# Kernel tuning notes

Hardware: AMD Instinct MI355X
Metric: run time of the kernel (lower is better)

The kernel has to match this reference:

```python
import jax, jax.numpy as jnp
import numpy as np

N = 16        # state dim n
M = 8         # control dim m
T = 50        # time_steps
DT = 0.01     # delta_t
SQRT_DT = DT ** 0.5
GAMMA = 0.1
SIGMA = 0.2
TAU = 0.5
H = 10        # hidden width of subnets
BATCH = 32768


def _mlp(params, x):
    W1, b1, W2, b2, W3, b3 = params
    h = jnp.tanh(x @ W1 + b1)
    h = jnp.tanh(h @ W2 + b2)
    return h @ W3 + b3


def setup_inputs() -> dict:
    key = jax.random.key(0)
    ks = jax.random.split(key, 32)

    def dense(k, i, o):
        return (jax.random.normal(k, (i, o), jnp.float32) / np.float32(np.sqrt(i)))

    inp = {
        'dw': jax.random.normal(ks[0], (T, BATCH, 1), jnp.float32) * SQRT_DT,
        'X0': jax.random.uniform(ks[1], (BATCH, N), jnp.float32),
        'A': dense(ks[2], N, N),
        'Bmat': dense(ks[3], N, M),
        'Cmat': dense(ks[4], N, N),
        'Dmat': dense(ks[5], N, M),
        # phi: (n+1) -> 10 -> 10 -> m
        'phi_W1': dense(ks[6], N + 1, H), 'phi_b1': jnp.zeros((H,), jnp.float32),
        'phi_W2': dense(ks[7], H, H),     'phi_b2': jnp.zeros((H,), jnp.float32),
        'phi_W3': dense(ks[8], H, M),     'phi_b3': jnp.zeros((M,), jnp.float32),
        # Z: (n+1) -> 10 -> 10 -> n
        'Z_W1': dense(ks[9], N + 1, H),   'Z_b1': jnp.zeros((H,), jnp.float32),
        'Z_W2': dense(ks[10], H, H),      'Z_b2': jnp.zeros((H,), jnp.float32),
        'Z_W3': dense(ks[11], H, N),      'Z_b3': jnp.zeros((N,), jnp.float32),
        # Y0: n -> 10 -> 10 -> n
        'Y0_W1': dense(ks[12], N, H),     'Y0_b1': jnp.zeros((H,), jnp.float32),
        'Y0_W2': dense(ks[13], H, H),     'Y0_b2': jnp.zeros((H,), jnp.float32),
        'Y0_W3': dense(ks[14], H, N),     'Y0_b3': jnp.zeros((N,), jnp.float32),
    }
    return inp


def reference(dw, X0, A, Bmat, Cmat, Dmat,
              phi_W1, phi_b1, phi_W2, phi_b2, phi_W3, phi_b3,
              Z_W1, Z_b1, Z_W2, Z_b2, Z_W3, Z_b3,
              Y0_W1, Y0_b1, Y0_W2, Y0_b2, Y0_W3, Y0_b3):
    phi_p = (phi_W1, phi_b1, phi_W2, phi_b2, phi_W3, phi_b3)
    Z_p = (Z_W1, Z_b1, Z_W2, Z_b2, Z_W3, Z_b3)
    Y0_p = (Y0_W1, Y0_b1, Y0_W2, Y0_b2, Y0_W3, Y0_b3)

    B = X0.shape[0]
    Y = _mlp(Y0_p, X0)                              # [B, n]
    t_grid = jnp.arange(T, dtype=X0.dtype) * DT     # [T]
    w_trap = jnp.ones((T,), X0.dtype).at[1:-1].set(2.0)  # trapezoid weights

    def step(carry, xs):
        X, Yc, lc = carry
        dwi, t, w = xs                              # dwi: [B,1]
        state = jnp.concatenate(
            [jnp.broadcast_to(t, (B, 1)).astype(X.dtype), X], axis=1)  # [B, n+1]
        Zv = _mlp(Z_p, state)                       # [B, n]
        u = _mlp(phi_p, state)                      # [B, m] (project = identity)
        # b_mult(M, x) == x @ M.T
        drift_X = X @ A.T + u @ Bmat.T + GAMMA      # [B, n]
        diffusion_X = X @ Cmat.T + u @ Dmat.T + SIGMA
        drift_Y = -(Yc @ A + Zv @ Cmat + X)         # f_x(X,u) = X
        # stop_recording branch: gradient of dH / pre_phi
        dH = Yc @ Bmat + Zv @ Dmat + u              # f_u(X,u) = u -> [B, m]
        pre_phi = jax.lax.stop_gradient(u - TAU * dH)
        Xn = X + drift_X * DT + dwi * diffusion_X
        Yn = Yc + drift_Y * DT + dwi * Zv
        lc = lc + 0.5 * DT * w * jnp.sum(jnp.square(u - pre_phi), axis=1)
        return (Xn, Yn, lc), None

    init = (X0, Y, jnp.zeros((B,), X0.dtype))
    (X, Y, loss_control), _ = jax.lax.scan(step, init, (dw, t_grid, w_trap))
    loss_bsde = jnp.sum(jnp.square(Y - X), axis=1)  # g_x(X) = X
    return jnp.stack([jnp.mean(loss_bsde), jnp.mean(loss_control)])
```

## Files before the change

### kernel.cpp

```cpp
#include <hip/hip_runtime.h>

namespace {

typedef float v4f __attribute__((ext_vector_type(4)));
typedef _Float16 half4 __attribute__((ext_vector_type(4)));
typedef __fp16 fp16x2 __attribute__((ext_vector_type(2)));
typedef unsigned int uint32;

constexpr int   kB     = 32768;
constexpr int   kT     = 50;
constexpr float kDT    = 0.01f;
constexpr float kGamma = 0.1f;
constexpr float kSigma = 0.2f;
constexpr float kTau   = 0.5f;
constexpr float kA     = 2.8853900817779268f;

constexpr int kNFrag      = 25;
constexpr int kFragDwords = kNFrag * 128;
constexpr int kBiasFloats = 13 * 16;

__device__ __forceinline__ float fexp2(float x) {
#if __has_builtin(__builtin_amdgcn_exp2f)
  return __builtin_amdgcn_exp2f(x);
#else
  return exp2f(x);
#endif
}

__device__ __forceinline__ float fact(float x) {
  return __builtin_amdgcn_rcpf(fexp2(x) + 1.0f);
}

__device__ __forceinline__ v4f act4(v4f a) {
  v4f r;
  r[0] = fact(a[0]); r[1] = fact(a[1]);
  r[2] = fact(a[2]); r[3] = fact(a[3]);
  return r;
}

__device__ __forceinline__ uint32 pk2rtn(float a, float b) {
  union { _Float16 h[2]; uint32 u; } z;
  z.h[0] = (_Float16)a; z.h[1] = (_Float16)b;
  return z.u;
}

__global__ __launch_bounds__(64) void prep_kernel(
    const float* __restrict__ A,   const float* __restrict__ Bm,
    const float* __restrict__ Cm,  const float* __restrict__ Dm,
    const float* __restrict__ pW1, const float* __restrict__ pb1,
    const float* __restrict__ pW2, const float* __restrict__ pb2,
    const float* __restrict__ pW3, const float* __restrict__ pb3,
    const float* __restrict__ zW1, const float* __restrict__ zb1,
    const float* __restrict__ zW2, const float* __restrict__ zb2,
    const float* __restrict__ zW3, const float* __restrict__ zb3,
    const float* __restrict__ yW1, const float* __restrict__ yb1,
    const float* __restrict__ yW2, const float* __restrict__ yb2,
    const float* __restrict__ yW3, const float* __restrict__ yb3,
    uint32* __restrict__ ws)
{
  const int tid = threadIdx.x;
  const int blk = blockIdx.x;

  auto sum10 = [](const float* W, int stride, int mm) {
    float s = 0.f;
#pragma unroll
    for (int j = 0; j < 10; ++j) s += W[j * stride + mm];
    return s;
  };

  if (blk < kNFrag) {
    const int m = tid & 15, q = tid >> 4;
    const int p = blk;

    auto comp = [&](const float* W1, const float* M, int ncol, int k,
                    float scale) -> float {
      if (m >= 10 || k >= ncol) return 0.f;
      float s = 0.f;
#pragma unroll
      for (int i = 0; i < 16; ++i) s += W1[(i + 1) * 10 + m] * M[i * ncol + k];
      return kA * scale * s;
    };

    auto wv = [&](int k) -> float {
      switch (p) {
        case 0:  return (m < 10) ? kA * yW1[k * 10 + m] : 0.f;
        case 1:  return (m < 10 && k < 10) ? -2.f * kA * yW2[k * 10 + m] : 0.f;
        case 2:  return (k < 10) ? -2.f * yW3[k * 16 + m] : 0.f;
        case 3:  return (m < 10) ? kA * zW1[(k + 1) * 10 + m] : 0.f;
        case 4:  return (m < 10) ? kA * pW1[(k + 1) * 10 + m] : 0.f;
        case 5:  return (m < 10 && k < 10) ? -2.f * kA * zW2[k * 10 + m] : 0.f;
        case 6:  return (m < 10 && k < 10) ? -2.f * kA * pW2[k * 10 + m] : 0.f;
        case 7:  return (k < 10) ? -2.f * zW3[k * 16 + m] : 0.f;
        case 8:  return (m < 8 && k < 10) ? -2.f * pW3[k * 8 + m] : 0.f;
        case 9:  return A[m * 16 + k];
        case 10: return (k < 8) ? Bm[m * 8 + k] : 0.f;
        case 11: return Cm[m * 16 + k];
        case 12: return (k < 8) ? Dm[m * 8 + k] : 0.f;
        case 13: return A[k * 16 + m];
        case 14: return Cm[k * 16 + m];
        case 15: return (m < 8) ? Bm[k * 8 + m] : 0.f;
        case 16: return (m < 8) ? Dm[k * 8 + m] : 0.f;
        case 17: return comp(zW1, A,  16, k, kDT);
        case 18: return comp(zW1, Cm, 16, k, 1.f);
        case 19: return comp(zW1, Bm,  8, k, kDT);
        case 20: return comp(zW1, Dm,  8, k, 1.f);
        case 21: return comp(pW1, A,  16, k, kDT);
        case 22: return comp(pW1, Cm, 16, k, 1.f);
        case 23: return comp(pW1, Bm,  8, k, kDT);
        case 24: return comp(pW1, Dm,  8, k, 1.f);
      }
      return 0.f;
    };

    const int k0 = 4 * q;
    ws[p * 128 + tid * 2]     = pk2rtn(wv(k0),     wv(k0 + 1));
    ws[p * 128 + tid * 2 + 1] = pk2rtn(wv(k0 + 2), wv(k0 + 3));
  } else {
    float* bsf = (float*)(ws + kFragDwords);
    auto sumx = [&](const float* W1, int mm) {
      float s = 0.f;
#pragma unroll
      for (int i = 0; i < 16; ++i) s += W1[(i + 1) * 10 + mm];
      return kA * s;
    };
    auto bval = [&](int a, int mm) -> float {
      const bool m10 = mm < 10;
      switch (a) {
        case 0:  return m10 ? kA * yb1[mm] : 0.f;
        case 1:  return m10 ? kA * (yb2[mm] + sum10(yW2, 10, mm)) : 0.f;
        case 2:  return yb3[mm] + sum10(yW3, 16, mm);
        case 3:  return m10 ? kA * (zb2[mm] + sum10(zW2, 10, mm)) : 0.f;
        case 4:  return m10 ? kA * (pb2[mm] + sum10(pW2, 10, mm)) : 0.f;
        case 5:  return zb3[mm] + sum10(zW3, 16, mm);
        case 6:  return (mm < 8) ? pb3[mm] + sum10(pW3, 8, mm) : 0.f;
        case 7:  return m10 ? kA * zW1[mm] : 0.f;
        case 8:  return m10 ? kA * zb1[mm] : 0.f;
        case 9:  return m10 ? kA * pW1[mm] : 0.f;
        case 10: return m10 ? kA * pb1[mm] : 0.f;
        case 11: return m10 ? sumx(zW1, mm) : 0.f;
        case 12: return m10 ? sumx(pW1, mm) : 0.f;
      }
      return 0.f;
    };
    for (int j = tid; j < kBiasFloats; j += 64) {
      bsf[j] = bval(j >> 4, j & 15);
    }
  }
}

__global__ __launch_bounds__(64)
__attribute__((amdgpu_waves_per_eu(2, 2)))
void bsde_kernel(const float* __restrict__ dw, const float* __restrict__ X0,
                 const uint32* __restrict__ wsu, float* __restrict__ out)
{
  const int lane = threadIdx.x;
  const int col  = lane & 15;
  const int quad = lane >> 4;
  const int e    = blockIdx.x * 16 + col;
  const int bq   = quad * 4;

  half4 af[kNFrag];
#pragma unroll
  for (int p = 0; p < kNFrag; ++p) {
    union { uint2 u; half4 h; } z;
    z.u = *(const uint2*)(wsu + p * 128 + lane * 2);
    af[p] = z.h;
  }

  const float* bsf = (const float*)(wsu + kFragDwords);
  const v4f c2z  = *(const v4f*)&bsf[3 * 16 + bq];
  const v4f c2p  = *(const v4f*)&bsf[4 * 16 + bq];
  const v4f c3z  = *(const v4f*)&bsf[5 * 16 + bq];
  const v4f c3p  = *(const v4f*)&bsf[6 * 16 + bq];
  const v4f vtz  = *(const v4f*)&bsf[7 * 16 + bq];
  const v4f vbz  = *(const v4f*)&bsf[8 * 16 + bq];
  const v4f vtp  = *(const v4f*)&bsf[9 * 16 + bq];
  const v4f vbp  = *(const v4f*)&bsf[10 * 16 + bq];
  const v4f w1sz = *(const v4f*)&bsf[11 * 16 + bq];
  const v4f w1sp = *(const v4f*)&bsf[12 * 16 + bq];

  auto pk4 = [](v4f a) -> half4 {
    union { fp16x2 p[2]; half4 h; } z;
    z.p[0] = __builtin_amdgcn_cvt_pkrtz(a[0], a[1]);
    z.p[1] = __builtin_amdgcn_cvt_pkrtz(a[2], a[3]);
    return z.h;
  };
  auto mm4 = [](half4 a, half4 b, v4f c) -> v4f {
    return __builtin_amdgcn_mfma_f32_16x16x16f16(a, b, c, 0, 0, 0);
  };

  const v4f gam4  = {kGamma, kGamma, kGamma, kGamma};
  const v4f sig4  = {kSigma, kSigma, kSigma, kSigma};
  const v4f zero4 = {0.f, 0.f, 0.f, 0.f};

  v4f x4 = *(const v4f*)&X0[e * 16 + bq];
  half4 xB = pk4(x4);
  v4f y4;
  {
    const v4f cy1 = *(const v4f*)&bsf[0 * 16 + bq];
    const v4f cy2 = *(const v4f*)&bsf[1 * 16 + bq];
    const v4f cy3 = *(const v4f*)&bsf[2 * 16 + bq];
    v4f h = mm4(af[0], xB, cy1);
    v4f g = mm4(af[1], pk4(act4(h)), cy2);
    y4    = mm4(af[2], pk4(act4(g)), cy3);
  }
  v4f hzp = mm4(af[3], xB, vbz);
  v4f hpp = mm4(af[4], xB, vbp);

  float dwv = dw[e];
  v4f xs0;
#pragma unroll
  for (int r = 0; r < 4; ++r) xs0[r] = x4[r] * dwv;
  half4 xDB = pk4(xs0);

  float lcp = 0.0f;

#pragma unroll 1
  for (int t = 0; t < kT; ++t) {
    const float dwn = (t < kT - 1) ? dw[(t + 1) * kB + e] : 0.0f;
    const float tvn = (float)(t + 1) * kDT;
    const float wt  = (t == 0 || t == kT - 1) ? 1.0f : 2.0f;

    half4 yB = pk4(y4);

    v4f dx1 = mm4(af[9],  xB, gam4);
    v4f fx1 = mm4(af[11], xB, sig4);
    v4f dy1 = mm4(af[13], yB, x4);
    v4f dh1 = mm4(af[15], yB, zero4);

    const float gs = kDT * kGamma + dwv * kSigma;
    v4f Cz, Cp;
#pragma unroll
    for (int r = 0; r < 4; ++r) {
      Cz[r] = vbz[r] + tvn * vtz[r] + gs * w1sz[r];
      Cp[r] = vbp[r] + tvn * vtp[r] + gs * w1sp[r];
    }
    v4f Ez = mm4(af[18], xDB, mm4(af[17], xB, mm4(af[3], xB, Cz)));
    v4f Ep = mm4(af[22], xDB, mm4(af[21], xB, mm4(af[4], xB, Cp)));

    v4f gz = mm4(af[5], pk4(act4(hzp)), c2z);
    v4f gp = mm4(af[6], pk4(act4(hpp)), c2p);
    v4f zv = mm4(af[7], pk4(act4(gz)), c3z);
    v4f uu = mm4(af[8], pk4(act4(gp)), c3p);

    half4 zB = pk4(zv);
    half4 uB = pk4(uu);

    v4f dx  = mm4(af[10], uB, dx1);
    v4f fx  = mm4(af[12], uB, fx1);
    v4f dy  = mm4(af[14], zB, dy1);
    v4f dh  = mm4(af[16], zB, dh1);
    v4f l1z = mm4(af[19], uB, Ez);
    v4f l2z = mm4(af[20], uB, zero4);
    v4f l1p = mm4(af[23], uB, Ep);
    v4f l2p = mm4(af[24], uB, zero4);

#pragma unroll
    for (int r = 0; r < 4; ++r) {
      hzp[r] = l1z[r] + dwv * l2z[r];
      hpp[r] = l1p[r] + dwv * l2p[r];
    }

    float ss = 0.0f;
    v4f Xn, Yn;
#pragma unroll
    for (int r = 0; r < 4; ++r) {
      Xn[r] = x4[r] + kDT * dx[r] + dwv * fx[r];
      Yn[r] = y4[r] - kDT * dy[r] + dwv * zv[r];
      float d = dh[r] + uu[r];
      ss += d * d;
    }
    lcp += (0.5f * kDT * kTau * kTau) * wt * ss;
    x4 = Xn; y4 = Yn;
    xB = pk4(x4);
    v4f xs;
#pragma unroll
    for (int r = 0; r < 4; ++r) xs[r] = x4[r] * dwn;
    xDB = pk4(xs);
    dwv = dwn;
  }

  float bp = 0.0f;
#pragma unroll
  for (int r = 0; r < 4; ++r) { float d = y4[r] - x4[r]; bp += d * d; }

#pragma unroll
  for (int s = 32; s > 0; s >>= 1) {
    bp  += __shfl_down(bp,  s, 64);
    lcp += __shfl_down(lcp, s, 64);
  }
  if (lane == 0) {
    atomicAdd(&out[0], bp  * (1.0f / (float)kB));
    atomicAdd(&out[1], lcp * (1.0f / (float)kB));
  }
}

}

extern "C" void kernel_launch(void* const* d_in, const int* in_sizes, int n_in,
                              void* d_out, int out_size, void* d_ws, size_t ws_size,
                              hipStream_t stream) {
  (void)in_sizes; (void)n_in; (void)ws_size; (void)out_size;

  const float* dw  = (const float*)d_in[0];
  const float* X0  = (const float*)d_in[1];
  const float* A   = (const float*)d_in[2];
  const float* Bm  = (const float*)d_in[3];
  const float* Cm  = (const float*)d_in[4];
  const float* Dm  = (const float*)d_in[5];
  const float* pW1 = (const float*)d_in[6];
  const float* pb1 = (const float*)d_in[7];
  const float* pW2 = (const float*)d_in[8];
  const float* pb2 = (const float*)d_in[9];
  const float* pW3 = (const float*)d_in[10];
  const float* pb3 = (const float*)d_in[11];
  const float* zW1 = (const float*)d_in[12];
  const float* zb1 = (const float*)d_in[13];
  const float* zW2 = (const float*)d_in[14];
  const float* zb2 = (const float*)d_in[15];
  const float* zW3 = (const float*)d_in[16];
  const float* zb3 = (const float*)d_in[17];
  const float* yW1 = (const float*)d_in[18];
  const float* yb1 = (const float*)d_in[19];
  const float* yW2 = (const float*)d_in[20];
  const float* yb2 = (const float*)d_in[21];
  const float* yW3 = (const float*)d_in[22];
  const float* yb3 = (const float*)d_in[23];
  float* out = (float*)d_out;
  unsigned int* ws = (unsigned int*)d_ws;

  (void)hipMemsetAsync(out, 0, 2 * sizeof(float), stream);

  prep_kernel<<<26, 64, 0, stream>>>(
      A, Bm, Cm, Dm,
      pW1, pb1, pW2, pb2, pW3, pb3,
      zW1, zb1, zW2, zb2, zW3, zb3,
      yW1, yb1, yW2, yb2, yW3, yb3, ws);

  bsde_kernel<<<kB / 16, 64, 0, stream>>>(dw, X0, ws, out);
}
```

Before: 199.4 us.

## Split Z and phi MLP chains across two waves with LDS exchange

Each block now runs two wavefronts. One evaluates the Z network and the Y/dH updates, the other evaluates the phi network and the X update. They exchange u and the new X through double-buffered shared memory with a barrier every time step. This drops the precomputed composite fragments (W1·A etc.) that previously let the next step's first layer be computed ahead, and halves the per-wave MFMA dependency chain. In exchange it adds a barrier per step, LDS traffic, and a critical path that is serialized again, since the first layer waits for the new X.

```diff
diff --git a/kernel.cpp b/kernel.cpp
--- a/kernel.cpp
+++ b/kernel.cpp
@@ -15,9 +15,9 @@
 constexpr float kTau   = 0.5f;
 constexpr float kA     = 2.8853900817779268f;
 
-constexpr int kNFrag      = 25;
+constexpr int kNFrag      = 17;
 constexpr int kFragDwords = kNFrag * 128;
-constexpr int kBiasFloats = 13 * 16;
+constexpr int kBiasFloats = 11 * 16;
 
 __device__ __forceinline__ float fexp2(float x) {
 #if __has_builtin(__builtin_amdgcn_exp2f)
@@ -71,15 +71,6 @@
   if (blk < kNFrag) {
     const int m = tid & 15, q = tid >> 4;
     const int p = blk;
-
-    auto comp = [&](const float* W1, const float* M, int ncol, int k,
-                    float scale) -> float {
-      if (m >= 10 || k >= ncol) return 0.f;
-      float s = 0.f;
-#pragma unroll
-      for (int i = 0; i < 16; ++i) s += W1[(i + 1) * 10 + m] * M[i * ncol + k];
-      return kA * scale * s;
-    };
 
     auto wv = [&](int k) -> float {
       switch (p) {
@@ -100,14 +91,6 @@
         case 14: return Cm[k * 16 + m];
         case 15: return (m < 8) ? Bm[k * 8 + m] : 0.f;
         case 16: return (m < 8) ? Dm[k * 8 + m] : 0.f;
-        case 17: return comp(zW1, A,  16, k, kDT);
-        case 18: return comp(zW1, Cm, 16, k, 1.f);
-        case 19: return comp(zW1, Bm,  8, k, kDT);
-        case 20: return comp(zW1, Dm,  8, k, 1.f);
-        case 21: return comp(pW1, A,  16, k, kDT);
-        case 22: return comp(pW1, Cm, 16, k, 1.f);
-        case 23: return comp(pW1, Bm,  8, k, kDT);
-        case 24: return comp(pW1, Dm,  8, k, 1.f);
       }
       return 0.f;
     };
@@ -117,12 +100,6 @@
     ws[p * 128 + tid * 2 + 1] = pk2rtn(wv(k0 + 2), wv(k0 + 3));
   } else {
     float* bsf = (float*)(ws + kFragDwords);
-    auto sumx = [&](const float* W1, int mm) {
-      float s = 0.f;
-#pragma unroll
-      for (int i = 0; i < 16; ++i) s += W1[(i + 1) * 10 + mm];
-      return kA * s;
-    };
     auto bval = [&](int a, int mm) -> float {
       const bool m10 = mm < 10;
       switch (a) {
@@ -137,8 +114,6 @@
         case 8:  return m10 ? kA * zb1[mm] : 0.f;
         case 9:  return m10 ? kA * pW1[mm] : 0.f;
         case 10: return m10 ? kA * pb1[mm] : 0.f;
-        case 11: return m10 ? sumx(zW1, mm) : 0.f;
-        case 12: return m10 ? sumx(pW1, mm) : 0.f;
       }
       return 0.f;
     };
@@ -148,36 +123,40 @@
   }
 }
 
-__global__ __launch_bounds__(64)
-__attribute__((amdgpu_waves_per_eu(2, 2)))
+__global__ __launch_bounds__(128)
+__attribute__((amdgpu_waves_per_eu(2, 4)))
 void bsde_kernel(const float* __restrict__ dw, const float* __restrict__ X0,
                  const uint32* __restrict__ wsu, float* __restrict__ out)
 {
-  const int lane = threadIdx.x;
+  const int tid  = threadIdx.x;
+  const int w    = tid >> 6;
+  const int lane = tid & 63;
   const int col  = lane & 15;
   const int quad = lane >> 4;
   const int e    = blockIdx.x * 16 + col;
   const int bq   = quad * 4;
 
-  half4 af[kNFrag];
-#pragma unroll
-  for (int p = 0; p < kNFrag; ++p) {
+  __shared__ float sx[2][64][4];
+  __shared__ float su[2][64][4];
+
+  auto ldfrag = [&](int p) -> half4 {
     union { uint2 u; half4 h; } z;
     z.u = *(const uint2*)(wsu + p * 128 + lane * 2);
-    af[p] = z.h;
-  }
-
+    return z.h;
+  };
   const float* bsf = (const float*)(wsu + kFragDwords);
-  const v4f c2z  = *(const v4f*)&bsf[3 * 16 + bq];
-  const v4f c2p  = *(const v4f*)&bsf[4 * 16 + bq];
-  const v4f c3z  = *(const v4f*)&bsf[5 * 16 + bq];
-  const v4f c3p  = *(const v4f*)&bsf[6 * 16 + bq];
-  const v4f vtz  = *(const v4f*)&bsf[7 * 16 + bq];
-  const v4f vbz  = *(const v4f*)&bsf[8 * 16 + bq];
-  const v4f vtp  = *(const v4f*)&bsf[9 * 16 + bq];
-  const v4f vbp  = *(const v4f*)&bsf[10 * 16 + bq];
-  const v4f w1sz = *(const v4f*)&bsf[11 * 16 + bq];
-  const v4f w1sp = *(const v4f*)&bsf[12 * 16 + bq];
+
+  const half4 aL1 = ldfrag(w ? 4 : 3);
+  const half4 aL2 = ldfrag(w ? 6 : 5);
+  const half4 aL3 = ldfrag(w ? 8 : 7);
+  const half4 aE0 = ldfrag(w ? 9 : 13);
+  const half4 aE1 = ldfrag(w ? 10 : 14);
+  const half4 aE2 = ldfrag(w ? 11 : 15);
+  const half4 aE3 = ldfrag(w ? 12 : 16);
+  const v4f c2 = *(const v4f*)&bsf[(w ? 4 : 3) * 16 + bq];
+  const v4f c3 = *(const v4f*)&bsf[(w ? 6 : 5) * 16 + bq];
+  const v4f vt = *(const v4f*)&bsf[(w ? 9 : 7) * 16 + bq];
+  const v4f vb = *(const v4f*)&bsf[(w ? 10 : 8) * 16 + bq];
 
   auto pk4 = [](v4f a) -> half4 {
     union { fp16x2 p[2]; half4 h; } z;
@@ -195,103 +174,89 @@
 
   v4f x4 = *(const v4f*)&X0[e * 16 + bq];
   half4 xB = pk4(x4);
-  v4f y4;
-  {
+  v4f y4 = zero4;
+  if (w == 0) {
+    const half4 a0 = ldfrag(0), a1 = ldfrag(1), a2 = ldfrag(2);
     const v4f cy1 = *(const v4f*)&bsf[0 * 16 + bq];
     const v4f cy2 = *(const v4f*)&bsf[1 * 16 + bq];
     const v4f cy3 = *(const v4f*)&bsf[2 * 16 + bq];
-    v4f h = mm4(af[0], xB, cy1);
-    v4f g = mm4(af[1], pk4(act4(h)), cy2);
-    y4    = mm4(af[2], pk4(act4(g)), cy3);
+    v4f h = mm4(a0, xB, cy1);
+    v4f g = mm4(a1, pk4(act4(h)), cy2);
+    y4    = mm4(a2, pk4(act4(g)), cy3);
   }
-  v4f hzp = mm4(af[3], xB, vbz);
-  v4f hpp = mm4(af[4], xB, vbp);
 
   float dwv = dw[e];
-  v4f xs0;
-#pragma unroll
-  for (int r = 0; r < 4; ++r) xs0[r] = x4[r] * dwv;
-  half4 xDB = pk4(xs0);
-
   float lcp = 0.0f;
+  int buf = 0;
 
 #pragma unroll 1
   for (int t = 0; t < kT; ++t) {
     const float dwn = (t < kT - 1) ? dw[(t + 1) * kB + e] : 0.0f;
-    const float tvn = (float)(t + 1) * kDT;
+    const float tv  = (float)t * kDT;
     const float wt  = (t == 0 || t == kT - 1) ? 1.0f : 2.0f;
 
+    v4f c1;
+#pragma unroll
+    for (int r = 0; r < 4; ++r) c1[r] = vb[r] + tv * vt[r];
+
+    v4f h = mm4(aL1, xB, c1);
+    v4f g = mm4(aL2, pk4(act4(h)), c2);
+    v4f o = mm4(aL3, pk4(act4(g)), c3);
+    half4 oB = pk4(o);
+
     half4 yB = pk4(y4);
-
-    v4f dx1 = mm4(af[9],  xB, gam4);
-    v4f fx1 = mm4(af[11], xB, sig4);
-    v4f dy1 = mm4(af[13], yB, x4);
-    v4f dh1 = mm4(af[15], yB, zero4);
-
-    const float gs = kDT * kGamma + dwv * kSigma;
-    v4f Cz, Cp;
-#pragma unroll
-    for (int r = 0; r < 4; ++r) {
-      Cz[r] = vbz[r] + tvn * vtz[r] + gs * w1sz[r];
-      Cp[r] = vbp[r] + tvn * vtp[r] + gs * w1sp[r];
-    }
-    v4f Ez = mm4(af[18], xDB, mm4(af[17], xB, mm4(af[3], xB, Cz)));
-    v4f Ep = mm4(af[22], xDB, mm4(af[21], xB, mm4(af[4], xB, Cp)));
-
-    v4f gz = mm4(af[5], pk4(act4(hzp)), c2z);
-    v4f gp = mm4(af[6], pk4(act4(hpp)), c2p);
-    v4f zv = mm4(af[7], pk4(act4(gz)), c3z);
-    v4f uu = mm4(af[8], pk4(act4(gp)), c3p);
-
-    half4 zB = pk4(zv);
-    half4 uB = pk4(uu);
-
-    v4f dx  = mm4(af[10], uB, dx1);
-    v4f fx  = mm4(af[12], uB, fx1);
-    v4f dy  = mm4(af[14], zB, dy1);
-    v4f dh  = mm4(af[16], zB, dh1);
-    v4f l1z = mm4(af[19], uB, Ez);
-    v4f l2z = mm4(af[20], uB, zero4);
-    v4f l1p = mm4(af[23], uB, Ep);
-    v4f l2p = mm4(af[24], uB, zero4);
-
-#pragma unroll
-    for (int r = 0; r < 4; ++r) {
-      hzp[r] = l1z[r] + dwv * l2z[r];
-      hpp[r] = l1p[r] + dwv * l2p[r];
-    }
-
-    float ss = 0.0f;
+    const half4 firstB = w ? xB : yB;
+    const v4f cA = w ? gam4 : x4;
+    const v4f cB = w ? sig4 : zero4;
+
+    v4f s1 = mm4(aE0, firstB, cA);
+    v4f p1 = mm4(aE1, oB, s1);
+    v4f s2 = mm4(aE2, firstB, cB);
+    v4f p2 = mm4(aE3, oB, s2);
+
     v4f Xn, Yn;
-#pragma unroll
-    for (int r = 0; r < 4; ++r) {
-      Xn[r] = x4[r] + kDT * dx[r] + dwv * fx[r];
-      Yn[r] = y4[r] - kDT * dy[r] + dwv * zv[r];
-      float d = dh[r] + uu[r];
-      ss += d * d;
-    }
-    lcp += (0.5f * kDT * kTau * kTau) * wt * ss;
-    x4 = Xn; y4 = Yn;
-    xB = pk4(x4);
-    v4f xs;
-#pragma unroll
-    for (int r = 0; r < 4; ++r) xs[r] = x4[r] * dwn;
-    xDB = pk4(xs);
+    if (w) {
+      *(v4f*)&su[buf][lane][0] = o;
+#pragma unroll
+      for (int r = 0; r < 4; ++r) Xn[r] = x4[r] + kDT * p1[r] + dwv * p2[r];
+      *(v4f*)&sx[buf][lane][0] = Xn;
+    } else {
+#pragma unroll
+      for (int r = 0; r < 4; ++r) Yn[r] = y4[r] - kDT * p1[r] + dwv * o[r];
+    }
+
+    __syncthreads();
+
+    if (w) {
+      x4 = Xn;
+      xB = pk4(x4);
+    } else {
+      const v4f uu = *(const v4f*)&su[buf][lane][0];
+      float ss = 0.0f;
+#pragma unroll
+      for (int r = 0; r < 4; ++r) { float d = p2[r] + uu[r]; ss += d * d; }
+      lcp += (0.5f * kDT * kTau * kTau) * wt * ss;
+      y4 = Yn;
+      x4 = *(const v4f*)&sx[buf][lane][0];
+      xB = pk4(x4);
+    }
     dwv = dwn;
+    buf ^= 1;
   }
 
-  float bp = 0.0f;
-#pragma unroll
-  for (int r = 0; r < 4; ++r) { float d = y4[r] - x4[r]; bp += d * d; }
-
-#pragma unroll
-  for (int s = 32; s > 0; s >>= 1) {
-    bp  += __shfl_down(bp,  s, 64);
-    lcp += __shfl_down(lcp, s, 64);
-  }
-  if (lane == 0) {
-    atomicAdd(&out[0], bp  * (1.0f / (float)kB));
-    atomicAdd(&out[1], lcp * (1.0f / (float)kB));
+  if (w == 0) {
+    float bp = 0.0f;
+#pragma unroll
+    for (int r = 0; r < 4; ++r) { float d = y4[r] - x4[r]; bp += d * d; }
+#pragma unroll
+    for (int s = 32; s > 0; s >>= 1) {
+      bp  += __shfl_down(bp,  s, 64);
+      lcp += __shfl_down(lcp, s, 64);
+    }
+    if (lane == 0) {
+      atomicAdd(&out[0], bp  * (1.0f / (float)kB));
+      atomicAdd(&out[1], lcp * (1.0f / (float)kB));
+    }
   }
 }
 
@@ -331,11 +296,11 @@
 
   (void)hipMemsetAsync(out, 0, 2 * sizeof(float), stream);
 
-  prep_kernel<<<26, 64, 0, stream>>>(
+  prep_kernel<<<kNFrag + 1, 64, 0, stream>>>(
       A, Bm, Cm, Dm,
       pW1, pb1, pW2, pb2, pW3, pb3,
       zW1, zb1, zW2, zb2, zW3, zb3,
       yW1, yb1, yW2, yb2, yW3, yb3, ws);
 
-  bsde_kernel<<<kB / 16, 64, 0, stream>>>(dw, X0, ws, out);
-}
+  bsde_kernel<<<kB / 16, 128, 0, stream>>>(dw, X0, ws, out);
+}
```

Measured after the change: 185.4 us. -7.0%, faster.
